# Kernel optimization log

Hardware: AMD Instinct MI355X
Metric: run time of the kernel (lower is better)

## Reference

```python
import jax, jax.numpy as jnp
import numpy as np

EMBED_DIM = 512
NUM_HEADS = 8
TGT_LEN = 2048
SRC_LEN = 2048
BSZ = 4
W_SCALE = 0.02  # keep pre-softmax logits in a sane range


def setup_inputs() -> dict:
    key = jax.random.key(0)
    ks = jax.random.split(key, 13)
    E = EMBED_DIM
    inp = {
        "query": jax.random.normal(ks[0], (TGT_LEN, BSZ, E), jnp.float32),
        "key": jax.random.normal(ks[1], (SRC_LEN, BSZ, E), jnp.float32),
        "value": jax.random.normal(ks[2], (SRC_LEN, BSZ, E), jnp.float32),
        "attn_mask": jax.random.normal(ks[3], (TGT_LEN, SRC_LEN), jnp.float32),
        # Linear params, torch layout: W is [out, in], y = x @ W.T + b
        "Wq": jax.random.normal(ks[4], (E, E), jnp.float32) * W_SCALE,
        "bq": jax.random.normal(ks[5], (E,), jnp.float32) * W_SCALE,
        "Wk": jax.random.normal(ks[6], (E, E), jnp.float32) * W_SCALE,
        "bk": jax.random.normal(ks[7], (E,), jnp.float32) * W_SCALE,
        "Wv": jax.random.normal(ks[8], (E, E), jnp.float32) * W_SCALE,
        "bv": jax.random.normal(ks[9], (E,), jnp.float32) * W_SCALE,
        "Wo": jax.random.normal(ks[10], (E, E), jnp.float32) * W_SCALE,
        "bo": jax.random.normal(ks[11], (E,), jnp.float32) * W_SCALE,
    }
    return inp


def reference(query, key, value, attn_mask, Wq, bq, Wk, bk, Wv, bv, Wo, bo):
    # QAT quant/dequant stubs are identity in float math; dropout p=0 (eval) is identity.
    T, B, E = query.shape
    S = key.shape[0]
    H = NUM_HEADS
    hd = E // H
    scale = hd ** (-0.5)

    q = query @ Wq.T + bq            # [T, B, E]
    k = key @ Wk.T + bk              # [S, B, E]
    v = value @ Wv.T + bv            # [S, B, E]

    q = q.reshape(T, B, H, hd) * scale
    k = k.reshape(S, B, H, hd)
    v = v.reshape(S, B, H, hd)

    # scores: [B, H, T, S]
    scores = jnp.einsum("tbhd,sbhd->bhts", q, k)
    scores = scores + attn_mask[None, None, :, :]  # mask_add.add (float mask)
    attn = jax.nn.softmax(scores, axis=-1)         # SegmentLUTSoftmax == softmax in float

    out = jnp.einsum("bhts,sbhd->tbhd", attn, v).reshape(T, B, E)
    out = out @ Wo.T + bo                          # out_proj

    # need_weights=True, average_attn_weights=True: mean over heads -> [B, T, S]
    attn_weights = jnp.sum(attn, axis=1) * (1.0 / H)
    return out, attn_weights
```

## Files before the change

### kernel.cpp

```cpp
#include <hip/hip_runtime.h>
#include <hip/hip_bf16.h>

#define T_LEN 2048
#define S_LEN 2048
#define BSZ   4
#define EMB   512
#define NHEAD 8
#define HDIM  64

using bf16x8 = __attribute__((ext_vector_type(8))) short;
using f32x4  = __attribute__((ext_vector_type(4))) float;

static __device__ __forceinline__ unsigned short f2bf(float x) {
    __hip_bfloat16 h = __float2bfloat16(x);
    return *reinterpret_cast<unsigned short*>(&h);
}
static __device__ __forceinline__ float bf2f(unsigned short u) {
    __hip_bfloat16 h;
    *reinterpret_cast<unsigned short*>(&h) = u;
    return __bfloat162float(h);
}

__global__ __launch_bounds__(256) void convert_split(const float* __restrict__ X,
                                                     unsigned short* __restrict__ Hi,
                                                     unsigned short* __restrict__ Lo,
                                                     int n4)
{
    const int stride = gridDim.x * 256;
    for (int i = blockIdx.x * 256 + threadIdx.x; i < n4; i += stride) {
        float4 v = ((const float4*)X)[i];
        unsigned short h0 = f2bf(v.x), h1 = f2bf(v.y), h2 = f2bf(v.z), h3 = f2bf(v.w);
        unsigned short g0 = f2bf(v.x - bf2f(h0)), g1 = f2bf(v.y - bf2f(h1));
        unsigned short g2 = f2bf(v.z - bf2f(h2)), g3 = f2bf(v.w - bf2f(h3));
        uint2 ph, pg;
        ph.x = (unsigned)h0 | ((unsigned)h1 << 16);
        ph.y = (unsigned)h2 | ((unsigned)h3 << 16);
        pg.x = (unsigned)g0 | ((unsigned)g1 << 16);
        pg.y = (unsigned)g2 | ((unsigned)g3 << 16);
        ((uint2*)Hi)[i] = ph;
        ((uint2*)Lo)[i] = pg;
    }
}

template <int MODE>
__global__ __launch_bounds__(256) void proj_mfma(
    const unsigned short* __restrict__ Xhi, const unsigned short* __restrict__ Xlo,
    const unsigned short* __restrict__ Whi, const unsigned short* __restrict__ Wlo,
    const float* __restrict__ bias,
    float* __restrict__ Yf, unsigned short* __restrict__ Yhi,
    unsigned short* __restrict__ Ylo, float scale)
{
    const int n0 = blockIdx.x * 64;
    const int m0 = blockIdx.y * 64;

    __shared__ unsigned short whs[64 * 64];
    __shared__ unsigned short wls[64 * 64];

    const int tid = threadIdx.x;
    const int w   = tid >> 6;
    const int l   = tid & 63;
    const int l4  = l >> 4, l15 = l & 15;
    const int sw  = (l & 7) << 4;
    char* whsb = (char*)whs;
    char* wlsb = (char*)wls;

    const int srow = tid >> 2;
    const int schk = tid & 3;
    const size_t wbase = (size_t)(n0 + srow) * 512 + schk * 16;
    const int stw = (srow * 128 + schk * 32) ^ ((srow & 7) << 4);

    const size_t xbase = (size_t)(m0 + w * 16 + l15) * 512 + l4 * 8;

    f32x4 acc[4];
    #pragma unroll
    for (int nb = 0; nb < 4; ++nb) { f32x4 z = {0.f, 0.f, 0.f, 0.f}; acc[nb] = z; }

    uint4 wh0 = *(const uint4*)(Whi + wbase);
    uint4 wh1 = *(const uint4*)(Whi + wbase + 8);
    uint4 wl0 = *(const uint4*)(Wlo + wbase);
    uint4 wl1 = *(const uint4*)(Wlo + wbase + 8);
    bf16x8 ah0 = *(const bf16x8*)(Xhi + xbase);
    bf16x8 ah1 = *(const bf16x8*)(Xhi + xbase + 32);
    bf16x8 al0 = *(const bf16x8*)(Xlo + xbase);
    bf16x8 al1 = *(const bf16x8*)(Xlo + xbase + 32);

    for (int c = 0; c < 8; ++c) {
        __syncthreads();
        *(uint4*)(whsb + stw)        = wh0;
        *(uint4*)(whsb + (stw ^ 16)) = wh1;
        *(uint4*)(wlsb + stw)        = wl0;
        *(uint4*)(wlsb + (stw ^ 16)) = wl1;
        __syncthreads();

        bf16x8 cah[2] = {ah0, ah1};
        bf16x8 cal[2] = {al0, al1};

        if (c < 7) {
            const size_t wb2 = wbase + (size_t)(c + 1) * 64;
            wh0 = *(const uint4*)(Whi + wb2);
            wh1 = *(const uint4*)(Whi + wb2 + 8);
            wl0 = *(const uint4*)(Wlo + wb2);
            wl1 = *(const uint4*)(Wlo + wb2 + 8);
            const size_t xb2 = xbase + (size_t)(c + 1) * 64;
            ah0 = *(const bf16x8*)(Xhi + xb2);
            ah1 = *(const bf16x8*)(Xhi + xb2 + 32);
            al0 = *(const bf16x8*)(Xlo + xb2);
            al1 = *(const bf16x8*)(Xlo + xb2 + 32);
        }

        #pragma unroll
        for (int kc = 0; kc < 2; ++kc) {
            #pragma unroll
            for (int nb = 0; nb < 4; ++nb) {
                const int off = (((nb * 16 + l15) * 128) + kc * 64 + l4 * 16) ^ sw;
                bf16x8 bh = *(const bf16x8*)(whsb + off);
                bf16x8 bl = *(const bf16x8*)(wlsb + off);
                acc[nb] = __builtin_amdgcn_mfma_f32_16x16x32_bf16(cah[kc], bh, acc[nb], 0, 0, 0);
                acc[nb] = __builtin_amdgcn_mfma_f32_16x16x32_bf16(cah[kc], bl, acc[nb], 0, 0, 0);
                acc[nb] = __builtin_amdgcn_mfma_f32_16x16x32_bf16(cal[kc], bh, acc[nb], 0, 0, 0);
            }
        }
    }

    #pragma unroll
    for (int nb = 0; nb < 4; ++nb)
        #pragma unroll
        for (int r = 0; r < 4; ++r) {
            const int m = m0 + w * 16 + l4 * 4 + r;
            const int n = n0 + nb * 16 + l15;
            const float y = (acc[nb][r] + bias[n]) * scale;
            const size_t idx = (size_t)m * 512 + n;
            if constexpr (MODE == 0) {
                Yf[idx] = y;
            } else if constexpr (MODE == 1) {
                const unsigned short hi = f2bf(y);
                Yhi[idx] = hi;
                Ylo[idx] = f2bf(y - bf2f(hi));
            } else {
                Yhi[idx] = f2bf(y);
            }
        }
}

__global__ __launch_bounds__(256) void transpose_v(const unsigned short* __restrict__ V,
                                                   unsigned short* __restrict__ Vt)
{
    const int s0 = blockIdx.x * 64;
    const int h  = blockIdx.y, b = blockIdx.z;
    __shared__ unsigned short tile[64][72];
    const int tid = threadIdx.x;
    {
        const int r = tid >> 2, c = (tid & 3) * 16;
        const unsigned short* src = V + ((size_t)(s0 + r) * BSZ + b) * EMB + h * HDIM + c;
        uint4 u0 = *(const uint4*)(src);
        uint4 u1 = *(const uint4*)(src + 8);
        *(uint4*)&tile[r][c]     = u0;
        *(uint4*)&tile[r][c + 8] = u1;
    }
    __syncthreads();
    {
        const int d = tid >> 2, sg = tid & 3;
        unsigned int w_[8];
        #pragma unroll
        for (int j = 0; j < 8; ++j) {
            unsigned int lo = tile[sg * 16 + 2 * j][d];
            unsigned int hi = tile[sg * 16 + 2 * j + 1][d];
            w_[j] = lo | (hi << 16);
        }
        uint4 o0 = {w_[0], w_[1], w_[2], w_[3]};
        uint4 o1 = {w_[4], w_[5], w_[6], w_[7]};
        unsigned short* dst = Vt + ((size_t)(b * NHEAD + h) * HDIM + d) * S_LEN + s0 + sg * 16;
        *(uint4*)dst       = o0;
        *(uint4*)(dst + 8) = o1;
    }
}

__global__ __launch_bounds__(256) void flash_fwd_mfma(
    const unsigned short* __restrict__ Qbf, const unsigned short* __restrict__ Kbf,
    const unsigned short* __restrict__ Vt,  const float* __restrict__ mask,
    unsigned short* __restrict__ Ohi, unsigned short* __restrict__ Olo,
    float* __restrict__ Lout)
{
    const int tt0 = blockIdx.x * 64;
    const int h   = blockIdx.y, b = blockIdx.z;

    __shared__ unsigned short ks[64 * 64];
    __shared__ unsigned short vs[64 * 64];
    __shared__ unsigned short pl[4][16 * 72];

    const int tid = threadIdx.x;
    const int w   = tid >> 6;
    const int l   = tid & 63;
    const int l4  = l >> 4, l15 = l & 15;
    const int sw  = (l & 7) << 4;

    char* ksb = (char*)ks;
    char* vsb = (char*)vs;

    bf16x8 qf[2];
    {
        const int t = tt0 + w * 16 + l15;
        const unsigned short* qp = Qbf + ((size_t)t * BSZ + b) * EMB + h * HDIM + l4 * 8;
        qf[0] = *(const bf16x8*)(qp);
        qf[1] = *(const bf16x8*)(qp + 32);
    }

    f32x4 oacc[4];
    #pragma unroll
    for (int nb = 0; nb < 4; ++nb) { f32x4 z = {0.f, 0.f, 0.f, 0.f}; oacc[nb] = z; }
    float l_r[4] = {0.f, 0.f, 0.f, 0.f};

    const int srow = tid >> 2;
    const int schk = tid & 3;
    const unsigned short* kcol = Kbf + (size_t)b * EMB + h * HDIM + schk * 16;
    const unsigned short* vrow = Vt + ((size_t)(b * NHEAD + h) * HDIM + srow) * S_LEN + schk * 16;
    const int stw = (srow * 128 + schk * 32) ^ ((srow & 7) << 4);

    const unsigned short* kp0 = kcol + (size_t)srow * BSZ * EMB;
    uint4 ka0 = *(const uint4*)(kp0);
    uint4 ka1 = *(const uint4*)(kp0 + 8);
    uint4 va0 = *(const uint4*)(vrow);
    uint4 va1 = *(const uint4*)(vrow + 8);

    for (int s0 = 0; s0 < S_LEN; s0 += 64) {
        __syncthreads();
        *(uint4*)(ksb + stw)        = ka0;
        *(uint4*)(ksb + (stw ^ 16)) = ka1;
        *(uint4*)(vsb + stw)        = va0;
        *(uint4*)(vsb + (stw ^ 16)) = va1;
        __syncthreads();

        if (s0 + 64 < S_LEN) {
            const unsigned short* kp2 = kcol + (size_t)(s0 + 64 + srow) * BSZ * EMB;
            ka0 = *(const uint4*)(kp2);
            ka1 = *(const uint4*)(kp2 + 8);
            va0 = *(const uint4*)(vrow + s0 + 64);
            va1 = *(const uint4*)(vrow + s0 + 64 + 8);
        }

        f32x4 sacc[4];
        #pragma unroll
        for (int nb = 0; nb < 4; ++nb) { f32x4 z = {0.f, 0.f, 0.f, 0.f}; sacc[nb] = z; }
        #pragma unroll
        for (int kc = 0; kc < 2; ++kc) {
            #pragma unroll
            for (int nb = 0; nb < 4; ++nb) {
                const int off = (((nb * 16 + l15) * 128) + kc * 64 + l4 * 16) ^ sw;
                bf16x8 kf = *(const bf16x8*)(ksb + off);
                sacc[nb] = __builtin_amdgcn_mfma_f32_16x16x32_bf16(qf[kc], kf, sacc[nb], 0, 0, 0);
            }
        }

        const float* mrow = mask + (size_t)(tt0 + w * 16 + l4 * 4) * S_LEN + s0 + l15;
        unsigned short pb[4][4];
        #pragma unroll
        for (int nb = 0; nb < 4; ++nb)
            #pragma unroll
            for (int r = 0; r < 4; ++r) {
                const float p = __expf(sacc[nb][r] + mrow[(size_t)r * S_LEN + nb * 16]);
                pb[nb][r] = f2bf(p);
                l_r[r] += p;
            }

        unsigned short* pw = pl[w];
        #pragma unroll
        for (int nb = 0; nb < 4; ++nb)
            #pragma unroll
            for (int r = 0; r < 4; ++r)
                pw[(l4 * 4 + r) * 72 + nb * 16 + l15] = pb[nb][r];

        bf16x8 pa0 = *(const bf16x8*)((char*)pw + (l15 * 144 + l4 * 16));
        bf16x8 pa1 = *(const bf16x8*)((char*)pw + (l15 * 144 + 64 + l4 * 16));
        #pragma unroll
        for (int nb = 0; nb < 4; ++nb) {
            const int off0 = (((nb * 16 + l15) * 128) + l4 * 16) ^ sw;
            bf16x8 vf0 = *(const bf16x8*)(vsb + off0);
            bf16x8 vf1 = *(const bf16x8*)(vsb + (off0 ^ 64));
            oacc[nb] = __builtin_amdgcn_mfma_f32_16x16x32_bf16(pa0, vf0, oacc[nb], 0, 0, 0);
            oacc[nb] = __builtin_amdgcn_mfma_f32_16x16x32_bf16(pa1, vf1, oacc[nb], 0, 0, 0);
        }
    }

    float linv[4];
    #pragma unroll
    for (int r = 0; r < 4; ++r) {
        float s = l_r[r];
        s += __shfl_xor(s, 1);
        s += __shfl_xor(s, 2);
        s += __shfl_xor(s, 4);
        s += __shfl_xor(s, 8);
        l_r[r] = s;
        linv[r] = 1.0f / s;
    }
    #pragma unroll
    for (int nb = 0; nb < 4; ++nb)
        #pragma unroll
        for (int r = 0; r < 4; ++r) {
            const int t = tt0 + w * 16 + l4 * 4 + r;
            const size_t idx = ((size_t)t * BSZ + b) * EMB + h * HDIM + nb * 16 + l15;
            const float y = oacc[nb][r] * linv[r];
            const unsigned short hi = f2bf(y);
            Ohi[idx] = hi;
            Olo[idx] = f2bf(y - bf2f(hi));
        }
    if (l15 == 0) {
        #pragma unroll
        for (int r = 0; r < 4; ++r) {
            const int t = tt0 + w * 16 + l4 * 4 + r;
            Lout[((size_t)b * NHEAD + h) * T_LEN + t] = l_r[r];
        }
    }
}

__global__ __launch_bounds__(256) void attn_weights_mfma(
    const unsigned short* __restrict__ Qhi, const unsigned short* __restrict__ Khi,
    const float* __restrict__ mask, const float* __restrict__ Lin,
    float* __restrict__ Wout)
{
    const int tt0 = blockIdx.x * 64;
    const int ss0 = blockIdx.y * 64;
    const int b   = blockIdx.z;

    __shared__ unsigned short khs[64 * 64];
    __shared__ float lls[NHEAD][64];

    const int tid = threadIdx.x;
    const int w   = tid >> 6;
    const int l   = tid & 63;
    const int l4  = l >> 4, l15 = l & 15;
    const int sw  = (l & 7) << 4;
    char* khsb = (char*)khs;

    #pragma unroll
    for (int i = tid; i < NHEAD * 64; i += 256) {
        const int hh = i >> 6, t2 = i & 63;
        lls[hh][t2] = 1.0f / Lin[(size_t)(b * NHEAD + hh) * T_LEN + tt0 + t2];
    }

    float msk[4][4];
    #pragma unroll
    for (int nb = 0; nb < 4; ++nb)
        #pragma unroll
        for (int r = 0; r < 4; ++r)
            msk[nb][r] = mask[(size_t)(tt0 + w * 16 + l4 * 4 + r) * S_LEN + ss0 + nb * 16 + l15];

    float wacc[4][4] = {};

    const int srow = tid >> 2;
    const int schk = tid & 3;
    const size_t kbase = ((size_t)(ss0 + srow) * BSZ + b) * EMB + schk * 16;
    const int stw = (srow * 128 + schk * 32) ^ ((srow & 7) << 4);
    const int t = tt0 + w * 16 + l15;
    const size_t qbase = ((size_t)t * BSZ + b) * EMB + l4 * 8;

    uint4 kh0 = *(const uint4*)(Khi + kbase);
    uint4 kh1 = *(const uint4*)(Khi + kbase + 8);

    for (int h = 0; h < NHEAD; ++h) {
        __syncthreads();
        *(uint4*)(khsb + stw)        = kh0;
        *(uint4*)(khsb + (stw ^ 16)) = kh1;
        __syncthreads();

        if (h < NHEAD - 1) {
            kh0 = *(const uint4*)(Khi + kbase + (h + 1) * HDIM);
            kh1 = *(const uint4*)(Khi + kbase + (h + 1) * HDIM + 8);
        }

        bf16x8 qh[2];
        qh[0] = *(const bf16x8*)(Qhi + qbase + h * HDIM);
        qh[1] = *(const bf16x8*)(Qhi + qbase + h * HDIM + 32);

        f32x4 sacc[4];
        #pragma unroll
        for (int nb = 0; nb < 4; ++nb) { f32x4 z = {0.f, 0.f, 0.f, 0.f}; sacc[nb] = z; }
        #pragma unroll
        for (int kc = 0; kc < 2; ++kc) {
            #pragma unroll
            for (int nb = 0; nb < 4; ++nb) {
                const int off = (((nb * 16 + l15) * 128) + kc * 64 + l4 * 16) ^ sw;
                bf16x8 kf = *(const bf16x8*)(khsb + off);
                sacc[nb] = __builtin_amdgcn_mfma_f32_16x16x32_bf16(qh[kc], kf, sacc[nb], 0, 0, 0);
            }
        }

        float lh[4];
        #pragma unroll
        for (int r = 0; r < 4; ++r)
            lh[r] = lls[h][w * 16 + l4 * 4 + r];
        #pragma unroll
        for (int nb = 0; nb < 4; ++nb)
            #pragma unroll
            for (int r = 0; r < 4; ++r)
                wacc[nb][r] += __expf(sacc[nb][r] + msk[nb][r]) * lh[r];
    }

    #pragma unroll
    for (int nb = 0; nb < 4; ++nb)
        #pragma unroll
        for (int r = 0; r < 4; ++r) {
            const size_t o = ((size_t)b * T_LEN + tt0 + w * 16 + l4 * 4 + r) * S_LEN
                           + ss0 + nb * 16 + l15;
            Wout[o] = wacc[nb][r] * (1.0f / NHEAD);
        }
}

extern "C" void kernel_launch(void* const* d_in, const int* in_sizes, int n_in,
                              void* d_out, int out_size, void* d_ws, size_t ws_size,
                              hipStream_t stream)
{
    const float* query = (const float*)d_in[0];
    const float* key   = (const float*)d_in[1];
    const float* value = (const float*)d_in[2];
    const float* mask  = (const float*)d_in[3];
    const float* Wq    = (const float*)d_in[4];
    const float* bq    = (const float*)d_in[5];
    const float* Wk    = (const float*)d_in[6];
    const float* bk    = (const float*)d_in[7];
    const float* Wv    = (const float*)d_in[8];
    const float* bv    = (const float*)d_in[9];
    const float* Wo    = (const float*)d_in[10];
    const float* bo    = (const float*)d_in[11];

    float* out = (float*)d_out;

    const size_t NQKV = (size_t)T_LEN * BSZ * EMB;
    const size_t NW   = (size_t)EMB * EMB;

    unsigned short* qhi = (unsigned short*)d_ws;
    unsigned short* khi = qhi + NQKV;
    unsigned short* vhi = khi + NQKV;
    unsigned short* wqh = vhi + NQKV;
    unsigned short* wql = wqh + NW;
    unsigned short* wkh = wql + NW;
    unsigned short* wkl = wkh + NW;
    unsigned short* wvh = wkl + NW;
    unsigned short* wvl = wvh + NW;
    unsigned short* woh = wvl + NW;
    unsigned short* wol = woh + NW;
    float* lb = (float*)(wol + NW);

    unsigned short* vt  = (unsigned short*)(out + NQKV);
    unsigned short* cxh = (unsigned short*)(out + NQKV + 3000000);
    unsigned short* cxl = (unsigned short*)(out + NQKV + 6000000);

    const dim3 gproj(8, 128);

    convert_split<<<256, 256, 0, stream>>>(Wq, wqh, wql, (int)(NW / 4));
    convert_split<<<256, 256, 0, stream>>>(Wk, wkh, wkl, (int)(NW / 4));
    convert_split<<<256, 256, 0, stream>>>(Wv, wvh, wvl, (int)(NW / 4));
    convert_split<<<256, 256, 0, stream>>>(Wo, woh, wol, (int)(NW / 4));

    convert_split<<<2048, 256, 0, stream>>>(query, cxh, cxl, (int)(NQKV / 4));
    proj_mfma<2><<<gproj, 256, 0, stream>>>(cxh, cxl, wqh, wql, bq,
                                            nullptr, qhi, nullptr, 0.125f);
    convert_split<<<2048, 256, 0, stream>>>(key, cxh, cxl, (int)(NQKV / 4));
    proj_mfma<2><<<gproj, 256, 0, stream>>>(cxh, cxl, wkh, wkl, bk,
                                            nullptr, khi, nullptr, 1.0f);
    convert_split<<<2048, 256, 0, stream>>>(value, cxh, cxl, (int)(NQKV / 4));
    proj_mfma<2><<<gproj, 256, 0, stream>>>(cxh, cxl, wvh, wvl, bv,
                                            nullptr, vhi, nullptr, 1.0f);

    transpose_v<<<dim3(S_LEN / 64, NHEAD, BSZ), 256, 0, stream>>>(vhi, vt);

    flash_fwd_mfma<<<dim3(T_LEN / 64, NHEAD, BSZ), 256, 0, stream>>>(
        qhi, khi, vt, mask, cxh, cxl, lb);

    proj_mfma<0><<<gproj, 256, 0, stream>>>(cxh, cxl, woh, wol, bo,
                                            out, nullptr, nullptr, 1.0f);

    attn_weights_mfma<<<dim3(T_LEN / 64, S_LEN / 64, BSZ), 256, 0, stream>>>(
        qhi, khi, mask, lb, out + NQKV);
}
```

Measured before the change: 281.2 us.

## Fuse input bf16 split into projections, batch weight conversion, transpose score MFMA

```diff
diff --git a/kernel.cpp b/kernel.cpp
--- a/kernel.cpp
+++ b/kernel.cpp
@@ -20,41 +20,48 @@
     *reinterpret_cast<unsigned short*>(&h) = u;
     return __bfloat162float(h);
 }
-
-__global__ __launch_bounds__(256) void convert_split(const float* __restrict__ X,
-                                                     unsigned short* __restrict__ Hi,
-                                                     unsigned short* __restrict__ Lo,
-                                                     int n4)
+static __device__ __forceinline__ unsigned int pk2(float a, float b) {
+    return (unsigned)f2bf(a) | ((unsigned)f2bf(b) << 16);
+}
+
+__global__ __launch_bounds__(256) void convert_w4(
+    const float* __restrict__ W0, const float* __restrict__ W1,
+    const float* __restrict__ W2, const float* __restrict__ W3,
+    unsigned short* __restrict__ Hi, unsigned short* __restrict__ Lo, int n4)
 {
+    const int z = blockIdx.y;
+    const float* X = (z == 0) ? W0 : (z == 1) ? W1 : (z == 2) ? W2 : W3;
+    unsigned short* H = Hi + (size_t)z * (size_t)EMB * EMB;
+    unsigned short* L = Lo + (size_t)z * (size_t)EMB * EMB;
     const int stride = gridDim.x * 256;
     for (int i = blockIdx.x * 256 + threadIdx.x; i < n4; i += stride) {
         float4 v = ((const float4*)X)[i];
         unsigned short h0 = f2bf(v.x), h1 = f2bf(v.y), h2 = f2bf(v.z), h3 = f2bf(v.w);
-        unsigned short g0 = f2bf(v.x - bf2f(h0)), g1 = f2bf(v.y - bf2f(h1));
-        unsigned short g2 = f2bf(v.z - bf2f(h2)), g3 = f2bf(v.w - bf2f(h3));
         uint2 ph, pg;
         ph.x = (unsigned)h0 | ((unsigned)h1 << 16);
         ph.y = (unsigned)h2 | ((unsigned)h3 << 16);
-        pg.x = (unsigned)g0 | ((unsigned)g1 << 16);
-        pg.y = (unsigned)g2 | ((unsigned)g3 << 16);
-        ((uint2*)Hi)[i] = ph;
-        ((uint2*)Lo)[i] = pg;
-    }
-}
-
-template <int MODE>
+        pg.x = pk2(v.x - bf2f(h0), v.y - bf2f(h1));
+        pg.y = pk2(v.z - bf2f(h2), v.w - bf2f(h3));
+        ((uint2*)H)[i] = ph;
+        ((uint2*)L)[i] = pg;
+    }
+}
+
+template <int MODE, bool XF32>
 __global__ __launch_bounds__(256) void proj_mfma(
+    const float* __restrict__ Xf,
     const unsigned short* __restrict__ Xhi, const unsigned short* __restrict__ Xlo,
     const unsigned short* __restrict__ Whi, const unsigned short* __restrict__ Wlo,
     const float* __restrict__ bias,
-    float* __restrict__ Yf, unsigned short* __restrict__ Yhi,
-    unsigned short* __restrict__ Ylo, float scale)
+    float* __restrict__ Yf, unsigned short* __restrict__ Yhi, float scale)
 {
     const int n0 = blockIdx.x * 64;
     const int m0 = blockIdx.y * 64;
 
     __shared__ unsigned short whs[64 * 64];
     __shared__ unsigned short wls[64 * 64];
+    __shared__ unsigned short xhs[XF32 ? 64 * 64 : 1];
+    __shared__ unsigned short xls[XF32 ? 64 * 64 : 1];
 
     const int tid = threadIdx.x;
     const int w   = tid >> 6;
@@ -63,14 +70,14 @@
     const int sw  = (l & 7) << 4;
     char* whsb = (char*)whs;
     char* wlsb = (char*)wls;
+    char* xhsb = (char*)xhs;
+    char* xlsb = (char*)xls;
 
     const int srow = tid >> 2;
     const int schk = tid & 3;
     const size_t wbase = (size_t)(n0 + srow) * 512 + schk * 16;
     const int stw = (srow * 128 + schk * 32) ^ ((srow & 7) << 4);
 
-    const size_t xbase = (size_t)(m0 + w * 16 + l15) * 512 + l4 * 8;
-
     f32x4 acc[4];
     #pragma unroll
     for (int nb = 0; nb < 4; ++nb) { f32x4 z = {0.f, 0.f, 0.f, 0.f}; acc[nb] = z; }
@@ -79,10 +86,22 @@
     uint4 wh1 = *(const uint4*)(Whi + wbase + 8);
     uint4 wl0 = *(const uint4*)(Wlo + wbase);
     uint4 wl1 = *(const uint4*)(Wlo + wbase + 8);
-    bf16x8 ah0 = *(const bf16x8*)(Xhi + xbase);
-    bf16x8 ah1 = *(const bf16x8*)(Xhi + xbase + 32);
-    bf16x8 al0 = *(const bf16x8*)(Xlo + xbase);
-    bf16x8 al1 = *(const bf16x8*)(Xlo + xbase + 32);
+
+    const size_t xfbase = (size_t)(m0 + srow) * 512 + schk * 16;
+    const size_t xbase  = (size_t)(m0 + w * 16 + l15) * 512 + l4 * 8;
+    float4 xp0, xp1, xp2, xp3;
+    bf16x8 ah0, ah1, al0, al1;
+    if constexpr (XF32) {
+        xp0 = *(const float4*)(Xf + xfbase);
+        xp1 = *(const float4*)(Xf + xfbase + 4);
+        xp2 = *(const float4*)(Xf + xfbase + 8);
+        xp3 = *(const float4*)(Xf + xfbase + 12);
+    } else {
+        ah0 = *(const bf16x8*)(Xhi + xbase);
+        ah1 = *(const bf16x8*)(Xhi + xbase + 32);
+        al0 = *(const bf16x8*)(Xlo + xbase);
+        al1 = *(const bf16x8*)(Xlo + xbase + 32);
+    }
 
     for (int c = 0; c < 8; ++c) {
         __syncthreads();
@@ -90,10 +109,38 @@
         *(uint4*)(whsb + (stw ^ 16)) = wh1;
         *(uint4*)(wlsb + stw)        = wl0;
         *(uint4*)(wlsb + (stw ^ 16)) = wl1;
+        if constexpr (XF32) {
+            uint4 H0, H1, L0, L1;
+            H0.x = pk2(xp0.x, xp0.y); H0.y = pk2(xp0.z, xp0.w);
+            H0.z = pk2(xp1.x, xp1.y); H0.w = pk2(xp1.z, xp1.w);
+            H1.x = pk2(xp2.x, xp2.y); H1.y = pk2(xp2.z, xp2.w);
+            H1.z = pk2(xp3.x, xp3.y); H1.w = pk2(xp3.z, xp3.w);
+            L0.x = pk2(xp0.x - bf2f(f2bf(xp0.x)), xp0.y - bf2f(f2bf(xp0.y)));
+            L0.y = pk2(xp0.z - bf2f(f2bf(xp0.z)), xp0.w - bf2f(f2bf(xp0.w)));
+            L0.z = pk2(xp1.x - bf2f(f2bf(xp1.x)), xp1.y - bf2f(f2bf(xp1.y)));
+            L0.w = pk2(xp1.z - bf2f(f2bf(xp1.z)), xp1.w - bf2f(f2bf(xp1.w)));
+            L1.x = pk2(xp2.x - bf2f(f2bf(xp2.x)), xp2.y - bf2f(f2bf(xp2.y)));
+            L1.y = pk2(xp2.z - bf2f(f2bf(xp2.z)), xp2.w - bf2f(f2bf(xp2.w)));
+            L1.z = pk2(xp3.x - bf2f(f2bf(xp3.x)), xp3.y - bf2f(f2bf(xp3.y)));
+            L1.w = pk2(xp3.z - bf2f(f2bf(xp3.z)), xp3.w - bf2f(f2bf(xp3.w)));
+            *(uint4*)(xhsb + stw)        = H0;
+            *(uint4*)(xhsb + (stw ^ 16)) = H1;
+            *(uint4*)(xlsb + stw)        = L0;
+            *(uint4*)(xlsb + (stw ^ 16)) = L1;
+        }
         __syncthreads();
 
-        bf16x8 cah[2] = {ah0, ah1};
-        bf16x8 cal[2] = {al0, al1};
+        bf16x8 cah[2], cal[2];
+        if constexpr (XF32) {
+            #pragma unroll
+            for (int kc = 0; kc < 2; ++kc) {
+                const int aoff = (((w * 16 + l15) * 128) + kc * 64 + l4 * 16) ^ sw;
+                cah[kc] = *(const bf16x8*)(xhsb + aoff);
+                cal[kc] = *(const bf16x8*)(xlsb + aoff);
+            }
+        } else {
+            cah[0] = ah0; cah[1] = ah1; cal[0] = al0; cal[1] = al1;
+        }
 
         if (c < 7) {
             const size_t wb2 = wbase + (size_t)(c + 1) * 64;
@@ -101,11 +148,19 @@
             wh1 = *(const uint4*)(Whi + wb2 + 8);
             wl0 = *(const uint4*)(Wlo + wb2);
             wl1 = *(const uint4*)(Wlo + wb2 + 8);
-            const size_t xb2 = xbase + (size_t)(c + 1) * 64;
-            ah0 = *(const bf16x8*)(Xhi + xb2);
-            ah1 = *(const bf16x8*)(Xhi + xb2 + 32);
-            al0 = *(const bf16x8*)(Xlo + xb2);
-            al1 = *(const bf16x8*)(Xlo + xb2 + 32);
+            if constexpr (XF32) {
+                const size_t xb2 = xfbase + (size_t)(c + 1) * 64;
+                xp0 = *(const float4*)(Xf + xb2);
+                xp1 = *(const float4*)(Xf + xb2 + 4);
+                xp2 = *(const float4*)(Xf + xb2 + 8);
+                xp3 = *(const float4*)(Xf + xb2 + 12);
+            } else {
+                const size_t xb2 = xbase + (size_t)(c + 1) * 64;
+                ah0 = *(const bf16x8*)(Xhi + xb2);
+                ah1 = *(const bf16x8*)(Xhi + xb2 + 32);
+                al0 = *(const bf16x8*)(Xlo + xb2);
+                al1 = *(const bf16x8*)(Xlo + xb2 + 32);
+            }
         }
 
         #pragma unroll
@@ -130,15 +185,8 @@
             const int n = n0 + nb * 16 + l15;
             const float y = (acc[nb][r] + bias[n]) * scale;
             const size_t idx = (size_t)m * 512 + n;
-            if constexpr (MODE == 0) {
-                Yf[idx] = y;
-            } else if constexpr (MODE == 1) {
-                const unsigned short hi = f2bf(y);
-                Yhi[idx] = hi;
-                Ylo[idx] = f2bf(y - bf2f(hi));
-            } else {
-                Yhi[idx] = f2bf(y);
-            }
+            if constexpr (MODE == 0) Yf[idx] = y;
+            else                     Yhi[idx] = f2bf(y);
         }
 }
 
@@ -186,7 +234,7 @@
 
     __shared__ unsigned short ks[64 * 64];
     __shared__ unsigned short vs[64 * 64];
-    __shared__ unsigned short pl[4][16 * 72];
+    __shared__ unsigned short pl[4][16 * 88];
 
     const int tid = threadIdx.x;
     const int w   = tid >> 6;
@@ -196,6 +244,7 @@
 
     char* ksb = (char*)ks;
     char* vsb = (char*)vs;
+    char* pwc = (char*)pl[w];
 
     bf16x8 qf[2];
     {
@@ -208,13 +257,15 @@
     f32x4 oacc[4];
     #pragma unroll
     for (int nb = 0; nb < 4; ++nb) { f32x4 z = {0.f, 0.f, 0.f, 0.f}; oacc[nb] = z; }
-    float l_r[4] = {0.f, 0.f, 0.f, 0.f};
+    float lsum = 0.f;
 
     const int srow = tid >> 2;
     const int schk = tid & 3;
     const unsigned short* kcol = Kbf + (size_t)b * EMB + h * HDIM + schk * 16;
     const unsigned short* vrow = Vt + ((size_t)(b * NHEAD + h) * HDIM + srow) * S_LEN + schk * 16;
     const int stw = (srow * 128 + schk * 32) ^ ((srow & 7) << 4);
+
+    const float* mrowp = mask + (size_t)(tt0 + w * 16 + l15) * S_LEN + l4 * 4;
 
     const unsigned short* kp0 = kcol + (size_t)srow * BSZ * EMB;
     uint4 ka0 = *(const uint4*)(kp0);
@@ -247,30 +298,26 @@
             for (int nb = 0; nb < 4; ++nb) {
                 const int off = (((nb * 16 + l15) * 128) + kc * 64 + l4 * 16) ^ sw;
                 bf16x8 kf = *(const bf16x8*)(ksb + off);
-                sacc[nb] = __builtin_amdgcn_mfma_f32_16x16x32_bf16(qf[kc], kf, sacc[nb], 0, 0, 0);
+                sacc[nb] = __builtin_amdgcn_mfma_f32_16x16x32_bf16(kf, qf[kc], sacc[nb], 0, 0, 0);
             }
         }
 
-        const float* mrow = mask + (size_t)(tt0 + w * 16 + l4 * 4) * S_LEN + s0 + l15;
-        unsigned short pb[4][4];
-        #pragma unroll
-        for (int nb = 0; nb < 4; ++nb)
-            #pragma unroll
-            for (int r = 0; r < 4; ++r) {
-                const float p = __expf(sacc[nb][r] + mrow[(size_t)r * S_LEN + nb * 16]);
-                pb[nb][r] = f2bf(p);
-                l_r[r] += p;
-            }
-
-        unsigned short* pw = pl[w];
-        #pragma unroll
-        for (int nb = 0; nb < 4; ++nb)
-            #pragma unroll
-            for (int r = 0; r < 4; ++r)
-                pw[(l4 * 4 + r) * 72 + nb * 16 + l15] = pb[nb][r];
-
-        bf16x8 pa0 = *(const bf16x8*)((char*)pw + (l15 * 144 + l4 * 16));
-        bf16x8 pa1 = *(const bf16x8*)((char*)pw + (l15 * 144 + 64 + l4 * 16));
+        #pragma unroll
+        for (int nb = 0; nb < 4; ++nb) {
+            float4 mk = *(const float4*)(mrowp + s0 + nb * 16);
+            const float p0 = __expf(sacc[nb][0] + mk.x);
+            const float p1 = __expf(sacc[nb][1] + mk.y);
+            const float p2 = __expf(sacc[nb][2] + mk.z);
+            const float p3 = __expf(sacc[nb][3] + mk.w);
+            lsum += (p0 + p1) + (p2 + p3);
+            uint2 pk;
+            pk.x = pk2(p0, p1);
+            pk.y = pk2(p2, p3);
+            *(uint2*)(pwc + l15 * 176 + nb * 32 + l4 * 8) = pk;
+        }
+
+        bf16x8 pa0 = *(const bf16x8*)(pwc + l15 * 176 + l4 * 16);
+        bf16x8 pa1 = *(const bf16x8*)(pwc + l15 * 176 + 64 + l4 * 16);
         #pragma unroll
         for (int nb = 0; nb < 4; ++nb) {
             const int off0 = (((nb * 16 + l15) * 128) + l4 * 16) ^ sw;
@@ -281,17 +328,14 @@
         }
     }
 
+    float lfull = lsum;
+    lfull += __shfl_xor(lfull, 16);
+    lfull += __shfl_xor(lfull, 32);
     float linv[4];
     #pragma unroll
-    for (int r = 0; r < 4; ++r) {
-        float s = l_r[r];
-        s += __shfl_xor(s, 1);
-        s += __shfl_xor(s, 2);
-        s += __shfl_xor(s, 4);
-        s += __shfl_xor(s, 8);
-        l_r[r] = s;
-        linv[r] = 1.0f / s;
-    }
+    for (int r = 0; r < 4; ++r)
+        linv[r] = 1.0f / __shfl(lfull, l4 * 4 + r);
+
     #pragma unroll
     for (int nb = 0; nb < 4; ++nb)
         #pragma unroll
@@ -303,13 +347,8 @@
             Ohi[idx] = hi;
             Olo[idx] = f2bf(y - bf2f(hi));
         }
-    if (l15 == 0) {
-        #pragma unroll
-        for (int r = 0; r < 4; ++r) {
-            const int t = tt0 + w * 16 + l4 * 4 + r;
-            Lout[((size_t)b * NHEAD + h) * T_LEN + t] = l_r[r];
-        }
-    }
+    if (l < 16)
+        Lout[((size_t)b * NHEAD + h) * T_LEN + tt0 + w * 16 + l] = lfull;
 }
 
 __global__ __launch_bounds__(256) void attn_weights_mfma(
@@ -337,21 +376,20 @@
         lls[hh][t2] = 1.0f / Lin[(size_t)(b * NHEAD + hh) * T_LEN + tt0 + t2];
     }
 
-    float msk[4][4];
-    #pragma unroll
-    for (int nb = 0; nb < 4; ++nb)
-        #pragma unroll
-        for (int r = 0; r < 4; ++r)
-            msk[nb][r] = mask[(size_t)(tt0 + w * 16 + l4 * 4 + r) * S_LEN + ss0 + nb * 16 + l15];
-
-    float wacc[4][4] = {};
+    float4 msk[4];
+    {
+        const float* mrowp = mask + (size_t)(tt0 + w * 16 + l15) * S_LEN + ss0 + l4 * 4;
+        #pragma unroll
+        for (int nb = 0; nb < 4; ++nb) msk[nb] = *(const float4*)(mrowp + nb * 16);
+    }
+
+    float4 wacc[4] = {};
 
     const int srow = tid >> 2;
     const int schk = tid & 3;
     const size_t kbase = ((size_t)(ss0 + srow) * BSZ + b) * EMB + schk * 16;
     const int stw = (srow * 128 + schk * 32) ^ ((srow & 7) << 4);
-    const int t = tt0 + w * 16 + l15;
-    const size_t qbase = ((size_t)t * BSZ + b) * EMB + l4 * 8;
+    const size_t qbase = ((size_t)(tt0 + w * 16 + l15) * BSZ + b) * EMB + l4 * 8;
 
     uint4 kh0 = *(const uint4*)(Khi + kbase);
     uint4 kh1 = *(const uint4*)(Khi + kbase + 8);
@@ -380,29 +418,27 @@
             for (int nb = 0; nb < 4; ++nb) {
                 const int off = (((nb * 16 + l15) * 128) + kc * 64 + l4 * 16) ^ sw;
                 bf16x8 kf = *(const bf16x8*)(khsb + off);
-                sacc[nb] = __builtin_amdgcn_mfma_f32_16x16x32_bf16(qh[kc], kf, sacc[nb], 0, 0, 0);
+                sacc[nb] = __builtin_amdgcn_mfma_f32_16x16x32_bf16(kf, qh[kc], sacc[nb], 0, 0, 0);
             }
         }
 
-        float lh[4];
-        #pragma unroll
-        for (int r = 0; r < 4; ++r)
-            lh[r] = lls[h][w * 16 + l4 * 4 + r];
-        #pragma unroll
-        for (int nb = 0; nb < 4; ++nb)
-            #pragma unroll
-            for (int r = 0; r < 4; ++r)
-                wacc[nb][r] += __expf(sacc[nb][r] + msk[nb][r]) * lh[r];
-    }
-
-    #pragma unroll
-    for (int nb = 0; nb < 4; ++nb)
-        #pragma unroll
-        for (int r = 0; r < 4; ++r) {
-            const size_t o = ((size_t)b * T_LEN + tt0 + w * 16 + l4 * 4 + r) * S_LEN
-                           + ss0 + nb * 16 + l15;
-            Wout[o] = wacc[nb][r] * (1.0f / NHEAD);
-        }
+        const float lh = lls[h][w * 16 + l15];
+        #pragma unroll
+        for (int nb = 0; nb < 4; ++nb) {
+            wacc[nb].x += __expf(sacc[nb][0] + msk[nb].x) * lh;
+            wacc[nb].y += __expf(sacc[nb][1] + msk[nb].y) * lh;
+            wacc[nb].z += __expf(sacc[nb][2] + msk[nb].z) * lh;
+            wacc[nb].w += __expf(sacc[nb][3] + msk[nb].w) * lh;
+        }
+    }
+
+    float* orow = Wout + ((size_t)b * T_LEN + tt0 + w * 16 + l15) * S_LEN + ss0 + l4 * 4;
+    #pragma unroll
+    for (int nb = 0; nb < 4; ++nb) {
+        float4 o = {wacc[nb].x * (1.0f / NHEAD), wacc[nb].y * (1.0f / NHEAD),
+                    wacc[nb].z * (1.0f / NHEAD), wacc[nb].w * (1.0f / NHEAD)};
+        *(float4*)(orow + nb * 16) = o;
+    }
 }
 
 extern "C" void kernel_launch(void* const* d_in, const int* in_sizes, int n_in,
@@ -430,15 +466,14 @@
     unsigned short* qhi = (unsigned short*)d_ws;
     unsigned short* khi = qhi + NQKV;
     unsigned short* vhi = khi + NQKV;
-    unsigned short* wqh = vhi + NQKV;
-    unsigned short* wql = wqh + NW;
-    unsigned short* wkh = wql + NW;
-    unsigned short* wkl = wkh + NW;
-    unsigned short* wvh = wkl + NW;
-    unsigned short* wvl = wvh + NW;
-    unsigned short* woh = wvl + NW;
-    unsigned short* wol = woh + NW;
-    float* lb = (float*)(wol + NW);
+    unsigned short* whb = vhi + NQKV;
+    unsigned short* wlb = whb + 4 * NW;
+    float* lb = (float*)(wlb + 4 * NW);
+
+    unsigned short* wqh = whb + 0 * NW, *wql = wlb + 0 * NW;
+    unsigned short* wkh = whb + 1 * NW, *wkl = wlb + 1 * NW;
+    unsigned short* wvh = whb + 2 * NW, *wvl = wlb + 2 * NW;
+    unsigned short* woh = whb + 3 * NW, *wol = wlb + 3 * NW;
 
     unsigned short* vt  = (unsigned short*)(out + NQKV);
     unsigned short* cxh = (unsigned short*)(out + NQKV + 3000000);
@@ -446,28 +481,22 @@
 
     const dim3 gproj(8, 128);
 
-    convert_split<<<256, 256, 0, stream>>>(Wq, wqh, wql, (int)(NW / 4));
-    convert_split<<<256, 256, 0, stream>>>(Wk, wkh, wkl, (int)(NW / 4));
-    convert_split<<<256, 256, 0, stream>>>(Wv, wvh, wvl, (int)(NW / 4));
-    convert_split<<<256, 256, 0, stream>>>(Wo, woh, wol, (int)(NW / 4));
-
-    convert_split<<<2048, 256, 0, stream>>>(query, cxh, cxl, (int)(NQKV / 4));
-    proj_mfma<2><<<gproj, 256, 0, stream>>>(cxh, cxl, wqh, wql, bq,
-                                            nullptr, qhi, nullptr, 0.125f);
-    convert_split<<<2048, 256, 0, stream>>>(key, cxh, cxl, (int)(NQKV / 4));
-    proj_mfma<2><<<gproj, 256, 0, stream>>>(cxh, cxl, wkh, wkl, bk,
-                                            nullptr, khi, nullptr, 1.0f);
-    convert_split<<<2048, 256, 0, stream>>>(value, cxh, cxl, (int)(NQKV / 4));
-    proj_mfma<2><<<gproj, 256, 0, stream>>>(cxh, cxl, wvh, wvl, bv,
-                                            nullptr, vhi, nullptr, 1.0f);
+    convert_w4<<<dim3(64, 4), 256, 0, stream>>>(Wq, Wk, Wv, Wo, whb, wlb, (int)(NW / 4));
+
+    proj_mfma<2, true><<<gproj, 256, 0, stream>>>(query, nullptr, nullptr, wqh, wql, bq,
+                                                  nullptr, qhi, 0.125f);
+    proj_mfma<2, true><<<gproj, 256, 0, stream>>>(key, nullptr, nullptr, wkh, wkl, bk,
+                                                  nullptr, khi, 1.0f);
+    proj_mfma<2, true><<<gproj, 256, 0, stream>>>(value, nullptr, nullptr, wvh, wvl, bv,
+                                                  nullptr, vhi, 1.0f);
 
     transpose_v<<<dim3(S_LEN / 64, NHEAD, BSZ), 256, 0, stream>>>(vhi, vt);
 
     flash_fwd_mfma<<<dim3(T_LEN / 64, NHEAD, BSZ), 256, 0, stream>>>(
         qhi, khi, vt, mask, cxh, cxl, lb);
 
-    proj_mfma<0><<<gproj, 256, 0, stream>>>(cxh, cxl, woh, wol, bo,
-                                            out, nullptr, nullptr, 1.0f);
+    proj_mfma<0, false><<<gproj, 256, 0, stream>>>(nullptr, cxh, cxl, woh, wol, bo,
+                                                   out, nullptr, 1.0f);
 
     attn_weights_mfma<<<dim3(T_LEN / 64, S_LEN / 64, BSZ), 256, 0, stream>>>(
         qhi, khi, mask, lb, out + NQKV);
```

Measured after the change: 256.9 us. -8.6%, faster.
